# Optimization experiments

Hardware: AMD Instinct MI355X
Metric: run time of the kernel (lower is better)

## Reference

```python
import jax, jax.numpy as jnp
import numpy as np

B, T_H, N, F_P = 16, 24, 256, 6
H, PRED_LEN, F_W = 64, 12, 4


def _build_static(coords):
    # haversine distance matrix -> gaussian kernel -> threshold (epsilon=0.5)
    lon, lat = coords[:, 0], coords[:, 1]
    dlon = lon[None, :] - lon[:, None]
    dlat = lat[None, :] - lat[:, None]
    a = (np.sin(np.radians(dlat / 2)) ** 2
         + np.cos(np.radians(lat[:, None])) * np.cos(np.radians(lat[None, :]))
         * np.sin(np.radians(dlon / 2)) ** 2)
    dist = 2.0 * 6371.0 * np.arcsin(np.sqrt(np.clip(a, 0.0, None)))
    std = dist.flatten().std()
    adj = np.exp(-np.square(dist / std))
    adj[adj < 0.5] = 0.0
    return adj.astype(np.float32)


def setup_inputs() -> dict:
    key = jax.random.key(0)
    ks = jax.random.split(key, 16)
    rng = np.random.default_rng(0)
    coords_np = np.stack([116.0 + rng.uniform(-1.0, 1.0, N),
                          40.0 + rng.uniform(-1.0, 1.0, N)], axis=1).astype(np.float32)
    s = 0.05
    scale_w = jnp.asarray([1.0, 360.0, 10.0, 1.0], jnp.float32)  # [_, dir(deg), speed, _]
    return {
        "history_pollution": jax.random.normal(ks[0], (B, T_H, N, F_P), jnp.float32),
        "history_weather": jax.random.uniform(ks[1], (B, T_H, F_W), jnp.float32) * scale_w,
        "static_adj": jnp.asarray(_build_static(coords_np)),
        "coords": jnp.asarray(coords_np),
        "w_gc1": jax.random.normal(ks[2], (H, F_P), jnp.float32) * s,
        "b_gc1": jax.random.normal(ks[3], (H,), jnp.float32) * s,
        "w_gc2": jax.random.normal(ks[4], (H, H), jnp.float32) * s,
        "b_gc2": jax.random.normal(ks[5], (H,), jnp.float32) * s,
        "w_ih": jax.random.normal(ks[6], (3 * H, H), jnp.float32) * s,
        "w_hh": jax.random.normal(ks[7], (3 * H, H), jnp.float32) * s,
        "b_ih": jax.random.normal(ks[8], (3 * H,), jnp.float32) * s,
        "b_hh": jax.random.normal(ks[9], (3 * H,), jnp.float32) * s,
        "w_m1": jax.random.normal(ks[10], (32, H), jnp.float32) * s,
        "b_m1": jax.random.normal(ks[11], (32,), jnp.float32) * s,
        "w_m2": jax.random.normal(ks[12], (F_P, 32), jnp.float32) * s,
        "b_m2": jax.random.normal(ks[13], (F_P,), jnp.float32) * s,
    }


def _forward(history_pollution, history_weather, static_adj, coords,
             w_gc1, b_gc1, w_gc2, b_gc2, w_ih, w_hh, b_ih, b_hh,
             w_m1, b_m1, w_m2, b_m2):
    Bs, Th, Ns, Fp = history_pollution.shape
    dt = history_pollution.dtype
    eye = jnp.eye(Ns, dtype=dt)
    # station pair angles: vecs[i,j] = coords[j] - coords[i]
    vecs = coords[None, :, :] - coords[:, None, :]
    ang = jnp.arctan2(vecs[..., 1], vecs[..., 0])  # [N,N]

    def gconv(x, adj, w, b):
        wt = adj + eye[None]                         # [B,N,N]
        d = 1.0 / (jnp.sqrt(wt.sum(-1)) + 1e-6)      # [B,N]
        norm = d[:, :, None] * wt * d[:, None, :]    # D^-1/2 W D^-1/2
        return jnp.einsum('bij,bjf->bif', norm, x) @ w.T + b

    def gcb(x, w_out, w_in):
        h1 = jax.nn.relu(gconv(x, w_out, w_gc1, b_gc1))
        return jax.nn.relu(gconv(h1, w_in, w_gc2, b_gc2))

    def gru(h, x):                                   # h,x: [B*N,H]
        gi = x @ w_ih.T + b_ih
        gh = h @ w_hh.T + b_hh
        i_r, i_z, i_n = jnp.split(gi, 3, axis=-1)
        h_r, h_z, h_n = jnp.split(gh, 3, axis=-1)
        r = jax.nn.sigmoid(i_r + h_r)
        z = jax.nn.sigmoid(i_z + h_z)
        n = jnp.tanh(i_n + r * h_n)
        return (1.0 - z) * n + z * h

    def mlp(x):
        return jax.nn.relu(x @ w_m1.T + b_m1) @ w_m2.T + b_m2

    def enc_step(carry, xs):
        h, _ = carry
        x_t, spd, wd = xs                            # [B,N,F],[B],[B]
        rad = jnp.deg2rad(wd)
        w_dyn = jnp.maximum(spd[:, None, None] * jnp.cos(ang[None] - rad[:, None, None]), 0.0)
        w_out = static_adj[None] * w_dyn             # [B,N,N]
        sf = gcb(x_t, w_out, jnp.swapaxes(w_out, 1, 2))
        h = gru(h, sf.reshape(Bs * Ns, -1))
        return (h, w_out), None

    h0 = jnp.zeros((Bs * Ns, w_hh.shape[1]), dt)
    xs = (jnp.moveaxis(history_pollution, 1, 0),      # [T,B,N,F]
          history_weather[:, :, 2].T,                 # wind speed [T,B]
          history_weather[:, :, 1].T)                 # wind dir   [T,B]
    (h, last_w_out), _ = jax.lax.scan(enc_step, (h0, jnp.zeros((Bs, Ns, Ns), dt)), xs)
    last_w_in = jnp.swapaxes(last_w_out, 1, 2)

    dec0 = mlp(h.reshape(Bs, Ns, -1))

    def dec_step(carry, _):
        h_c, x = carry
        sf = gcb(x, last_w_out, last_w_in)
        h_c = gru(h_c, sf.reshape(Bs * Ns, -1))
        pred = mlp(h_c.reshape(Bs, Ns, -1))
        return (h_c, pred), pred

    _, preds = jax.lax.scan(dec_step, (h, dec0), None, length=PRED_LEN)
    return jnp.moveaxis(preds, 0, 1)                  # [B, pred_len, N, F_P]


def reference(history_pollution, history_weather, static_adj, coords,
              w_gc1, b_gc1, w_gc2, b_gc2, w_ih, w_hh, b_ih, b_hh,
              w_m1, b_m1, w_m2, b_m2):
    return _forward(history_pollution, history_weather, static_adj, coords,
                    w_gc1, b_gc1, w_gc2, b_gc2, w_ih, w_hh, b_ih, b_hh,
                    w_m1, b_m1, w_m2, b_m2)
```

## Files before the change

### kernel.cpp

```cpp
#include <hip/hip_runtime.h>
#include <math.h>

#define Bsz 16
#define Tt 24
#define Nn 256
#define Fp 6
#define Hh 64
#define PredL 12
#define Fw 4
#define M1 32
#define TCHUNK 8
#define DEG2RAD 0.017453292519943295f
#define IDX2(t, b) ((t) * Bsz + (b))

__global__ __launch_bounds__(256) void k_prep(
    const float* __restrict__ coords, const float* __restrict__ adj,
    const float* __restrict__ wgc2, const float* __restrict__ wih,
    const float* __restrict__ whh,  const float* __restrict__ wm1,
    const float* __restrict__ wm2,
    float2* __restrict__ pk,
    float* __restrict__ wgc2T, float* __restrict__ wm1T, float* __restrict__ wm2T,
    float4* __restrict__ wihP, float4* __restrict__ whhP) {
  int tid = threadIdx.x;
  if (blockIdx.x < Nn) {
    int i = blockIdx.x;
    int j = tid;
    float dx = coords[2 * j]     - coords[2 * i];
    float dy = coords[2 * j + 1] - coords[2 * i + 1];
    float ang = atan2f(dy, dx);
    float a = adj[i * Nn + j];
    pk[i * Nn + j] = make_float2(a * cosf(ang), a * sinf(ang));
    return;
  }
  for (int idx = tid; idx < Hh * Hh; idx += 256) {
    int g = idx / Hh, k = idx % Hh;
    wgc2T[k * Hh + g] = wgc2[g * Hh + k];
  }
  for (int idx = tid; idx < M1 * Hh; idx += 256) {
    int m = idx / Hh, k = idx % Hh;
    wm1T[k * M1 + m] = wm1[m * Hh + k];
  }
  for (int idx = tid; idx < Fp * M1; idx += 256) {
    int f = idx / M1, m = idx % M1;
    wm2T[m * Fp + f] = wm2[f * M1 + m];
  }
  for (int idx = tid; idx < Hh * 64; idx += 256) {
    int k = idx >> 6, lane = idx & 63;
    wihP[idx] = make_float4(wih[(0 * 64 + lane) * Hh + k],
                            wih[(1 * 64 + lane) * Hh + k],
                            wih[(2 * 64 + lane) * Hh + k], 0.f);
    whhP[idx] = make_float4(whh[(0 * 64 + lane) * Hh + k],
                            whh[(1 * 64 + lane) * Hh + k],
                            whh[(2 * 64 + lane) * Hh + k], 0.f);
  }
}

__global__ __launch_bounds__(256) void k_deg(
    const float* __restrict__ hw, const float2* __restrict__ pk,
    float* __restrict__ dbuf, float* __restrict__ ebuf) {
  int q  = blockIdx.x & 3;
  int tb = blockIdx.x >> 2;
  int t = tb / Bsz, b = tb % Bsz;
  float spd = hw[(b * Tt + t) * Fw + 2];
  float rad = hw[(b * Tt + t) * Fw + 1] * DEG2RAD;
  float cr = cosf(rad), sr = sinf(rad);
  int w = threadIdx.x >> 6, lane = threadIdx.x & 63;
  for (int m = 0; m < 16; ++m) {
    int i = q * 64 + w * 16 + m;
    float rs = 0.f, cs = 0.f;
#pragma unroll
    for (int c = 0; c < 4; ++c) {
      int j = lane + 64 * c;
      float2 pv = pk[i * Nn + j];
      float val = spd * (pv.x * cr + pv.y * sr);
      rs += fmaxf(val, 0.f);
      cs += (j == i) ? fmaxf(val, 0.f) : fmaxf(-val, 0.f);
    }
#pragma unroll
    for (int off = 32; off; off >>= 1) {
      rs += __shfl_xor(rs, off);
      cs += __shfl_xor(cs, off);
    }
    if (lane == 0) {
      dbuf[IDX2(t, b) * Nn + i] = 1.f / (sqrtf(rs + 1.f) + 1e-6f);
      ebuf[IDX2(t, b) * Nn + i] = 1.f / (sqrtf(cs + 1.f) + 1e-6f);
    }
  }
}

__global__ __launch_bounds__(256) void k_enc(
    const float2* __restrict__ pk, const float* __restrict__ hp,
    const float* __restrict__ hw,
    const float* __restrict__ dbuf, const float* __restrict__ ebuf,
    const float* __restrict__ wgc1, const float* __restrict__ bgc1,
    const float* __restrict__ wgc2T, const float* __restrict__ bgc2,
    float* __restrict__ sf_all) {
  __shared__ __align__(16) float u_s[Nn * 8];
  __shared__ __align__(16) float h1_s[Nn * 68];
  int tb = blockIdx.x, t = tb / Bsz, b = tb % Bsz;
  int i = threadIdx.x;
  float spd = hw[(b * Tt + t) * Fw + 2];
  float rad = hw[(b * Tt + t) * Fw + 1] * DEG2RAD;
  float cr = cosf(rad), sr = sinf(rad);
  const float* drow = dbuf + IDX2(t, b) * Nn;
  float di = drow[i];
  float ei = ebuf[IDX2(t, b) * Nn + i];
  const float* xsrc = hp + (long)(b * Tt + t) * Nn * Fp;
  for (int idx = i; idx < Nn * Fp; idx += 256) {
    int j = idx / Fp, f = idx - j * Fp;
    u_s[j * 8 + f] = drow[j] * xsrc[idx];
  }
  u_s[i * 8 + 6] = 0.f;
  u_s[i * 8 + 7] = 0.f;
  __syncthreads();

  float a0 = 0.f, a1 = 0.f, a2 = 0.f, a3 = 0.f, a4 = 0.f, a5 = 0.f;
#pragma unroll 4
  for (int j = 0; j < Nn; ++j) {
    float2 pv = pk[j * Nn + i];
    float vji = spd * (pv.x * cr + pv.y * sr);
    float wout = (j == i) ? fmaxf(vji, 0.f) : fmaxf(-vji, 0.f);
    float4 ul = *(const float4*)&u_s[j * 8];
    float4 uh = *(const float4*)&u_s[j * 8 + 4];
    a0 += wout * ul.x; a1 += wout * ul.y; a2 += wout * ul.z;
    a3 += wout * ul.w; a4 += wout * uh.x; a5 += wout * uh.y;
  }
  float y0 = di * (a0 + u_s[i * 8 + 0]);
  float y1 = di * (a1 + u_s[i * 8 + 1]);
  float y2v = di * (a2 + u_s[i * 8 + 2]);
  float y3 = di * (a3 + u_s[i * 8 + 3]);
  float y4 = di * (a4 + u_s[i * 8 + 4]);
  float y5 = di * (a5 + u_s[i * 8 + 5]);

#pragma unroll
  for (int g4 = 0; g4 < 16; ++g4) {
    float4 hv;
#pragma unroll
    for (int q = 0; q < 4; ++q) {
      int g = g4 * 4 + q;
      float v = bgc1[g] + wgc1[g * Fp + 0] * y0 + wgc1[g * Fp + 1] * y1 +
                wgc1[g * Fp + 2] * y2v + wgc1[g * Fp + 3] * y3 +
                wgc1[g * Fp + 4] * y4 + wgc1[g * Fp + 5] * y5;
      v = fmaxf(v, 0.f) * ei;
      ((float*)&hv)[q] = v;
    }
    *(float4*)&h1_s[i * 68 + g4 * 4] = hv;
  }
  __syncthreads();

  float z[64];
#pragma unroll
  for (int k = 0; k < 64; ++k) z[k] = 0.f;
#pragma unroll 2
  for (int j = 0; j < Nn; ++j) {
    float2 pv = pk[j * Nn + i];
    float vji = spd * (pv.x * cr + pv.y * sr);
    float wf = fmaxf(vji, 0.f) + ((j == i) ? 1.f : 0.f);
#pragma unroll
    for (int g4 = 0; g4 < 16; ++g4) {
      float4 h4 = *(const float4*)&h1_s[j * 68 + g4 * 4];
      z[g4 * 4 + 0] += wf * h4.x;
      z[g4 * 4 + 1] += wf * h4.y;
      z[g4 * 4 + 2] += wf * h4.z;
      z[g4 * 4 + 3] += wf * h4.w;
    }
  }
#pragma unroll
  for (int k = 0; k < 64; ++k) z[k] *= ei;
  __syncthreads();

#pragma unroll
  for (int c = 0; c < 4; ++c) {
    float s[16];
#pragma unroll
    for (int q = 0; q < 16; ++q) s[q] = bgc2[c * 16 + q];
#pragma unroll
    for (int k = 0; k < 64; ++k) {
      float zk = z[k];
#pragma unroll
      for (int q = 0; q < 16; ++q) s[q] += wgc2T[k * Hh + c * 16 + q] * zk;
    }
#pragma unroll
    for (int q4 = 0; q4 < 4; ++q4) {
      float4 sv = make_float4(fmaxf(s[q4 * 4 + 0], 0.f), fmaxf(s[q4 * 4 + 1], 0.f),
                              fmaxf(s[q4 * 4 + 2], 0.f), fmaxf(s[q4 * 4 + 3], 0.f));
      *(float4*)&h1_s[i * 68 + c * 16 + q4 * 4] = sv;
    }
  }
  __syncthreads();
  long base = (long)IDX2(t, b) * Nn * Hh;
  for (int idx = i; idx < Nn * 16; idx += 256) {
    int j = idx >> 4, g4 = idx & 15;
    *(float4*)&sf_all[base + j * Hh + g4 * 4] = *(const float4*)&h1_s[j * 68 + g4 * 4];
  }
}

__global__ __launch_bounds__(256) void k_gi(
    const float* __restrict__ sf_all, const float4* __restrict__ wihP,
    const float* __restrict__ bih, float* __restrict__ gi, int t0) {
  __shared__ float sf_c[4][16][64];
  int tid = threadIdx.x, w = tid >> 6, lane = tid & 63;
  int rowc0 = blockIdx.x * 64 + w * 16;
  long rowg0 = (long)t0 * (Bsz * Nn) + rowc0;
#pragma unroll
  for (int rr = 0; rr < 16; ++rr)
    sf_c[w][rr][lane] = sf_all[(rowg0 + rr) * Hh + lane];
  float bi_r = bih[lane], bi_z = bih[64 + lane], bi_n = bih[128 + lane];
  float ar[16], az[16], an[16];
#pragma unroll
  for (int rr = 0; rr < 16; ++rr) { ar[rr] = bi_r; az[rr] = bi_z; an[rr] = bi_n; }
#pragma unroll 2
  for (int kb = 0; kb < 16; ++kb) {
    int k0 = kb * 4;
    float4 wi0 = wihP[(k0 + 0) * 64 + lane];
    float4 wi1 = wihP[(k0 + 1) * 64 + lane];
    float4 wi2 = wihP[(k0 + 2) * 64 + lane];
    float4 wi3 = wihP[(k0 + 3) * 64 + lane];
#pragma unroll
    for (int rr = 0; rr < 16; ++rr) {
      const float4 s4 = *(const float4*)&sf_c[w][rr][k0];
      ar[rr] += s4.x * wi0.x + s4.y * wi1.x + s4.z * wi2.x + s4.w * wi3.x;
      az[rr] += s4.x * wi0.y + s4.y * wi1.y + s4.z * wi2.y + s4.w * wi3.y;
      an[rr] += s4.x * wi0.z + s4.y * wi1.z + s4.z * wi2.z + s4.w * wi3.z;
    }
  }
#pragma unroll
  for (int rr = 0; rr < 16; ++rr) {
    long rowc = rowc0 + rr;
    gi[(rowc * 3 + 0) * 64 + lane] = ar[rr];
    gi[(rowc * 3 + 1) * 64 + lane] = az[rr];
    gi[(rowc * 3 + 2) * 64 + lane] = an[rr];
  }
}

__global__ __launch_bounds__(256) void k_gru_scan4(
    const float* __restrict__ gi, const float4* __restrict__ whhP,
    const float* __restrict__ bhh, float* __restrict__ hstate,
    int t0, int nt) {
  __shared__ float h_s[16][64];
  int b = blockIdx.x >> 4;
  int i0 = (blockIdx.x & 15) * 16;
  int tid = threadIdx.x, w = tid >> 6, lane = tid & 63;
  float bh_r = bhh[lane], bh_z = bhh[64 + lane], bh_n = bhh[128 + lane];
  float h_reg[4];
#pragma unroll
  for (int rr = 0; rr < 4; ++rr) {
    float hv = (t0 == 0) ? 0.f
                         : hstate[((long)b * Nn + i0 + w * 4 + rr) * Hh + lane];
    h_reg[rr] = hv;
    h_s[w * 4 + rr][lane] = hv;
  }
  for (int tl = 0; tl < nt; ++tl) {
    long rbase = ((long)tl * Bsz + b) * Nn + i0 + w * 4;
    float gr[4], gz[4], gn[4], hr[4], hz[4], hn[4];
#pragma unroll
    for (int rr = 0; rr < 4; ++rr) {
      gr[rr] = gi[((rbase + rr) * 3 + 0) * 64 + lane];
      gz[rr] = gi[((rbase + rr) * 3 + 1) * 64 + lane];
      gn[rr] = gi[((rbase + rr) * 3 + 2) * 64 + lane];
      hr[rr] = bh_r; hz[rr] = bh_z; hn[rr] = bh_n;
    }
#pragma unroll 4
    for (int kb = 0; kb < 16; ++kb) {
      int k0 = kb * 4;
      float4 wh0 = whhP[(k0 + 0) * 64 + lane];
      float4 wh1 = whhP[(k0 + 1) * 64 + lane];
      float4 wh2 = whhP[(k0 + 2) * 64 + lane];
      float4 wh3 = whhP[(k0 + 3) * 64 + lane];
#pragma unroll
      for (int rr = 0; rr < 4; ++rr) {
        const float4 h4 = *(const float4*)&h_s[w * 4 + rr][k0];
        hr[rr] += h4.x * wh0.x + h4.y * wh1.x + h4.z * wh2.x + h4.w * wh3.x;
        hz[rr] += h4.x * wh0.y + h4.y * wh1.y + h4.z * wh2.y + h4.w * wh3.y;
        hn[rr] += h4.x * wh0.z + h4.y * wh1.z + h4.z * wh2.z + h4.w * wh3.z;
      }
    }
#pragma unroll
    for (int rr = 0; rr < 4; ++rr) {
      float rg = 1.f / (1.f + expf(-(gr[rr] + hr[rr])));
      float zg = 1.f / (1.f + expf(-(gz[rr] + hz[rr])));
      float ng = tanhf(gn[rr] + rg * hn[rr]);
      float hv = (1.f - zg) * ng + zg * h_reg[rr];
      h_reg[rr] = hv;
      h_s[w * 4 + rr][lane] = hv;
    }
  }
#pragma unroll
  for (int rr = 0; rr < 4; ++rr)
    hstate[((long)b * Nn + i0 + w * 4 + rr) * Hh + lane] = h_reg[rr];
}

__global__ __launch_bounds__(256) void k_norm_dec(
    const float* __restrict__ hw, const float2* __restrict__ pk,
    const float* __restrict__ dbuf, const float* __restrict__ ebuf,
    float* __restrict__ A1d, float* __restrict__ A2d) {
  int b = blockIdx.x >> 8;
  int i = blockIdx.x & 255;
  int j = threadIdx.x;
  float spd = hw[(b * Tt + (Tt - 1)) * Fw + 2];
  float rad = hw[(b * Tt + (Tt - 1)) * Fw + 1] * DEG2RAD;
  float cr = cosf(rad), sr = sinf(rad);
  const float* drow = dbuf + IDX2(Tt - 1, b) * Nn;
  const float* erow = ebuf + IDX2(Tt - 1, b) * Nn;
  float2 pv = pk[i * Nn + j];
  float val = spd * (pv.x * cr + pv.y * sr);
  float dlt = (j == i) ? 1.f : 0.f;
  float wout = fmaxf(val, 0.f);
  float win  = (j == i) ? wout : fmaxf(-val, 0.f);
  A1d[((long)b * Nn + i) * Nn + j] = drow[i] * (wout + dlt) * drow[j];
  A2d[((long)b * Nn + i) * Nn + j] = erow[i] * (win + dlt) * erow[j];
}

__global__ __launch_bounds__(256) void k_dec0(
    const float* __restrict__ hstate,
    const float* __restrict__ wm1T, const float* __restrict__ bm1,
    const float* __restrict__ wm2T, const float* __restrict__ bm2,
    float* __restrict__ xnext) {
  const int RPB = 16;
  __shared__ float h_lds[RPB][Hh];
  __shared__ float u_lds[RPB][M1];
  int r0 = blockIdx.x * RPB;
  int tid = threadIdx.x;
#pragma unroll
  for (int c = 0; c < (RPB * Hh) / 256; ++c) {
    int idx = tid + c * 256;
    h_lds[idx >> 6][idx & 63] = hstate[(long)r0 * Hh + idx];
  }
  __syncthreads();
#pragma unroll
  for (int rep = 0; rep < 2; ++rep) {
    int idx = tid + rep * 256;
    int row = idx >> 5, m = idx & 31;
    float um = bm1[m];
    for (int k = 0; k < Hh; ++k) um += wm1T[k * M1 + m] * h_lds[row][k];
    u_lds[row][m] = fmaxf(um, 0.f);
  }
  __syncthreads();
  if (tid < RPB * Fp) {
    int row = tid / Fp, f = tid % Fp;
    float pf = bm2[f];
#pragma unroll
    for (int m = 0; m < M1; ++m) pf += wm2T[m * Fp + f] * u_lds[row][m];
    xnext[(r0 + row) * Fp + f] = pf;
  }
}

__global__ __launch_bounds__(256) void k_dstep_A(
    const float* __restrict__ xb, const float* __restrict__ A1d,
    const float* __restrict__ wgc1, const float* __restrict__ bgc1,
    float* __restrict__ h1d) {
  __shared__ float x_lds[Nn * Fp];
  int b = blockIdx.x >> 4;
  int i0 = (blockIdx.x & 15) * 16;
  int tid = threadIdx.x, w = tid >> 6, lane = tid & 63;
  const float* xsrc = xb + (long)b * Nn * Fp;
#pragma unroll
  for (int c = 0; c < 6; ++c) x_lds[tid + 256 * c] = xsrc[tid + 256 * c];
  __syncthreads();
#pragma unroll
  for (int rr = 0; rr < 4; ++rr) {
    int i = i0 + w * 4 + rr;
    const float* arow = A1d + ((long)b * Nn + i) * Nn;
    float acc[Fp] = {0.f, 0.f, 0.f, 0.f, 0.f, 0.f};
#pragma unroll
    for (int c = 0; c < 4; ++c) {
      int j = lane + 64 * c;
      float wt = arow[j];
#pragma unroll
      for (int f = 0; f < Fp; ++f) acc[f] += wt * x_lds[j * Fp + f];
    }
#pragma unroll
    for (int f = 0; f < Fp; ++f) {
#pragma unroll
      for (int off = 32; off; off >>= 1) acc[f] += __shfl_xor(acc[f], off);
    }
    float hv = bgc1[lane];
#pragma unroll
    for (int f = 0; f < Fp; ++f) hv += wgc1[lane * Fp + f] * acc[f];
    h1d[((long)b * Nn + i) * Hh + lane] = fmaxf(hv, 0.f);
  }
}

__global__ __launch_bounds__(256) void k_dstep_B(
    const float* __restrict__ A2d, const float* __restrict__ h1d,
    const float* __restrict__ wgc2T, const float* __restrict__ bgc2,
    const float4* __restrict__ wihP, const float4* __restrict__ whhP,
    const float* __restrict__ bih, const float* __restrict__ bhh,
    float* __restrict__ hstate,
    const float* __restrict__ wm1T, const float* __restrict__ bm1,
    const float* __restrict__ wm2T, const float* __restrict__ bm2,
    float* __restrict__ outp, float* __restrict__ xnext, int p) {
  __shared__ __align__(16) float wvT[Nn * 20];
  __shared__ float red[4][16][Hh];
  __shared__ float y2[16][Hh];
  __shared__ float sf_s[16][Hh];
  __shared__ float h_s[16][Hh];
  __shared__ float hn_lds[16][Hh];
  __shared__ float u_lds[16][M1];
  int b = blockIdx.x >> 4;
  int i0 = (blockIdx.x & 15) * 16;
  int tid = threadIdx.x, w = tid >> 6, lane = tid & 63;

#pragma unroll
  for (int r = 0; r < 16; ++r)
    wvT[tid * 20 + r] = A2d[((long)b * Nn + i0 + r) * Nn + tid];
  float hp_reg[4];
#pragma unroll
  for (int rr = 0; rr < 4; ++rr) {
    hp_reg[rr] = hstate[((long)b * Nn + i0 + w * 4 + rr) * Hh + lane];
    h_s[w * 4 + rr][lane] = hp_reg[rr];
  }
  __syncthreads();

  float acc[16];
#pragma unroll
  for (int r = 0; r < 16; ++r) acc[r] = 0.f;
  const float* h1b = h1d + (long)b * Nn * Hh;
#pragma unroll 4
  for (int jj = 0; jj < 64; ++jj) {
    int j = w * 64 + jj;
    float hv = h1b[j * Hh + lane];
    const float4* wp = (const float4*)(wvT + j * 20);
    float4 w0 = wp[0], w1 = wp[1], w2 = wp[2], w3 = wp[3];
    acc[0] += w0.x * hv; acc[1] += w0.y * hv; acc[2] += w0.z * hv; acc[3] += w0.w * hv;
    acc[4] += w1.x * hv; acc[5] += w1.y * hv; acc[6] += w1.z * hv; acc[7] += w1.w * hv;
    acc[8] += w2.x * hv; acc[9] += w2.y * hv; acc[10] += w2.z * hv; acc[11] += w2.w * hv;
    acc[12] += w3.x * hv; acc[13] += w3.y * hv; acc[14] += w3.z * hv; acc[15] += w3.w * hv;
  }
#pragma unroll
  for (int r = 0; r < 16; ++r) red[w][r][lane] = acc[r];
  __syncthreads();
#pragma unroll
  for (int rr = 0; rr < 4; ++rr) {
    int r = w * 4 + rr;
    y2[r][lane] = red[0][r][lane] + red[1][r][lane] + red[2][r][lane] + red[3][r][lane];
  }
  {
    float a0 = bgc2[lane], a1 = a0, a2 = a0, a3 = a0;
    for (int k = 0; k < Hh; ++k) {
      float wk = wgc2T[k * Hh + lane];
      a0 += wk * y2[w * 4 + 0][k];
      a1 += wk * y2[w * 4 + 1][k];
      a2 += wk * y2[w * 4 + 2][k];
      a3 += wk * y2[w * 4 + 3][k];
    }
    sf_s[w * 4 + 0][lane] = fmaxf(a0, 0.f);
    sf_s[w * 4 + 1][lane] = fmaxf(a1, 0.f);
    sf_s[w * 4 + 2][lane] = fmaxf(a2, 0.f);
    sf_s[w * 4 + 3][lane] = fmaxf(a3, 0.f);
  }

  float hn_reg[4];
  {
    float bi_r = bih[lane], bi_z = bih[64 + lane], bi_n = bih[128 + lane];
    float bh_r = bhh[lane], bh_z = bhh[64 + lane], bh_n = bhh[128 + lane];
    float gir[4], giz[4], gin[4], ghr[4], ghz[4], ghn[4];
#pragma unroll
    for (int rr = 0; rr < 4; ++rr) {
      gir[rr] = bi_r; giz[rr] = bi_z; gin[rr] = bi_n;
      ghr[rr] = bh_r; ghz[rr] = bh_z; ghn[rr] = bh_n;
    }
#pragma unroll 4
    for (int kb = 0; kb < 16; ++kb) {
      int k0 = kb * 4;
      float4 wi[4], wh[4];
#pragma unroll
      for (int q = 0; q < 4; ++q) {
        wi[q] = wihP[(k0 + q) * 64 + lane];
        wh[q] = whhP[(k0 + q) * 64 + lane];
      }
#pragma unroll
      for (int rr = 0; rr < 4; ++rr) {
        const float4 s4 = *(const float4*)&sf_s[w * 4 + rr][k0];
        const float4 h4 = *(const float4*)&h_s[w * 4 + rr][k0];
        gir[rr] += s4.x * wi[0].x + s4.y * wi[1].x + s4.z * wi[2].x + s4.w * wi[3].x;
        giz[rr] += s4.x * wi[0].y + s4.y * wi[1].y + s4.z * wi[2].y + s4.w * wi[3].y;
        gin[rr] += s4.x * wi[0].z + s4.y * wi[1].z + s4.z * wi[2].z + s4.w * wi[3].z;
        ghr[rr] += h4.x * wh[0].x + h4.y * wh[1].x + h4.z * wh[2].x + h4.w * wh[3].x;
        ghz[rr] += h4.x * wh[0].y + h4.y * wh[1].y + h4.z * wh[2].y + h4.w * wh[3].y;
        ghn[rr] += h4.x * wh[0].z + h4.y * wh[1].z + h4.z * wh[2].z + h4.w * wh[3].z;
      }
    }
#pragma unroll
    for (int rr = 0; rr < 4; ++rr) {
      float rg = 1.f / (1.f + expf(-(gir[rr] + ghr[rr])));
      float zg = 1.f / (1.f + expf(-(giz[rr] + ghz[rr])));
      float ng = tanhf(gin[rr] + rg * ghn[rr]);
      hn_reg[rr] = (1.f - zg) * ng + zg * hp_reg[rr];
      hstate[((long)b * Nn + i0 + w * 4 + rr) * Hh + lane] = hn_reg[rr];
      hn_lds[w * 4 + rr][lane] = hn_reg[rr];
    }
  }
  __syncthreads();
#pragma unroll
  for (int rep = 0; rep < 2; ++rep) {
    int idx = tid + rep * 256;
    int row = idx >> 5, m = idx & 31;
    float um = bm1[m];
    for (int k = 0; k < Hh; ++k) um += wm1T[k * M1 + m] * hn_lds[row][k];
    u_lds[row][m] = fmaxf(um, 0.f);
  }
  __syncthreads();
  if (tid < 16 * Fp) {
    int row = tid / Fp, f = tid % Fp;
    float pf = bm2[f];
#pragma unroll
    for (int m = 0; m < M1; ++m) pf += wm2T[m * Fp + f] * u_lds[row][m];
    int i = i0 + row;
    outp[(((long)b * PredL + p) * Nn + i) * Fp + f] = pf;
    xnext[((long)b * Nn + i) * Fp + f] = pf;
  }
}

extern "C" void kernel_launch(void* const* d_in, const int* in_sizes, int n_in,
                              void* d_out, int out_size, void* d_ws, size_t ws_size,
                              hipStream_t stream) {
  const float* hp     = (const float*)d_in[0];
  const float* hw     = (const float*)d_in[1];
  const float* adj    = (const float*)d_in[2];
  const float* coords = (const float*)d_in[3];
  const float* wgc1   = (const float*)d_in[4];
  const float* bgc1   = (const float*)d_in[5];
  const float* wgc2   = (const float*)d_in[6];
  const float* bgc2   = (const float*)d_in[7];
  const float* wih    = (const float*)d_in[8];
  const float* whh    = (const float*)d_in[9];
  const float* bih    = (const float*)d_in[10];
  const float* bhh    = (const float*)d_in[11];
  const float* wm1    = (const float*)d_in[12];
  const float* bm1    = (const float*)d_in[13];
  const float* wm2    = (const float*)d_in[14];
  const float* bm2    = (const float*)d_in[15];
  float* out = (float*)d_out;

  float* w = (float*)d_ws;
  float2* pk    = (float2*)w; w += Nn * Nn * 2;
  float* dbuf   = w; w += Tt * Bsz * Nn;
  float* ebuf   = w; w += Tt * Bsz * Nn;
  float* hstate = w; w += Bsz * Nn * Hh;
  float* sf_all = w; w += (long)Tt * Bsz * Nn * Hh;
  float* gi_ch  = w; w += (long)TCHUNK * Bsz * Nn * 3 * 64;
  float* h1d    = w; w += Bsz * Nn * Hh;
  float* xb0    = w; w += Bsz * Nn * Fp;
  float* xb1    = w; w += Bsz * Nn * Fp;
  float* A1d    = w; w += Bsz * Nn * Nn;
  float* A2d    = w; w += Bsz * Nn * Nn;
  float* wgc2T  = w; w += Hh * Hh;
  float* wm1T   = w; w += Hh * M1;
  float* wm2T   = w; w += M1 * Fp;
  float4* wihP  = (float4*)w; w += Hh * 64 * 4;
  float4* whhP  = (float4*)w; w += Hh * 64 * 4;

  k_prep<<<Nn + 1, 256, 0, stream>>>(coords, adj, wgc2, wih, whh, wm1, wm2,
                                     pk, wgc2T, wm1T, wm2T, wihP, whhP);
  k_deg<<<Tt * Bsz * 4, 256, 0, stream>>>(hw, pk, dbuf, ebuf);

  k_enc<<<Tt * Bsz, 256, 0, stream>>>(pk, hp, hw, dbuf, ebuf,
                                      wgc1, bgc1, wgc2T, bgc2, sf_all);

  for (int s = 0; s < Tt / TCHUNK; ++s) {
    int t0 = s * TCHUNK;
    k_gi<<<(TCHUNK * Bsz * Nn) / 64, 256, 0, stream>>>(sf_all, wihP, bih,
                                                       gi_ch, t0);
    k_gru_scan4<<<Bsz * 16, 256, 0, stream>>>(gi_ch, whhP, bhh, hstate,
                                              t0, TCHUNK);
  }

  k_norm_dec<<<Bsz * Nn, 256, 0, stream>>>(hw, pk, dbuf, ebuf, A1d, A2d);
  k_dec0<<<Bsz * Nn / 16, 256, 0, stream>>>(hstate, wm1T, bm1, wm2T, bm2, xb0);

  for (int p = 0; p < PredL; ++p) {
    float* xin  = (p & 1) ? xb1 : xb0;
    float* xout = (p & 1) ? xb0 : xb1;
    k_dstep_A<<<Bsz * 16, 256, 0, stream>>>(xin, A1d, wgc1, bgc1, h1d);
    k_dstep_B<<<Bsz * 16, 256, 0, stream>>>(
        A2d, h1d, wgc2T, bgc2, wihP, whhP, bih, bhh, hstate,
        wm1T, bm1, wm2T, bm2, out, xout, p);
  }
}
```

Baseline: 738.5 us.

## Fuse degree computation into encoder and register-tile the second graph aggregation

Drops the separate degree kernel and computes the row and column degree normalisers inside each encoder block, keeping only the last timestep's values for the decoder. The second aggregation is restructured so each thread accumulates an 8x8 tile of nodes by features with vectorised pk loads, replacing the per-thread 64-wide accumulator. The final linear layer writes straight to global memory, and the encoder chunk size rises from 8 to 12, which means fewer gi/GRU launches but a larger gi buffer. Degrees are now recomputed in every block, the diagonal term is handled separately, and launch bounds now ask for two blocks per CU.

```diff
diff --git a/kernel.cpp b/kernel.cpp
--- a/kernel.cpp
+++ b/kernel.cpp
@@ -9,7 +9,7 @@
 #define PredL 12
 #define Fw 4
 #define M1 32
-#define TCHUNK 8
+#define TCHUNK 12
 #define DEG2RAD 0.017453292519943295f
 #define IDX2(t, b) ((t) * Bsz + (b))
 
@@ -55,143 +55,174 @@
   }
 }
 
-__global__ __launch_bounds__(256) void k_deg(
-    const float* __restrict__ hw, const float2* __restrict__ pk,
-    float* __restrict__ dbuf, float* __restrict__ ebuf) {
-  int q  = blockIdx.x & 3;
-  int tb = blockIdx.x >> 2;
-  int t = tb / Bsz, b = tb % Bsz;
-  float spd = hw[(b * Tt + t) * Fw + 2];
-  float rad = hw[(b * Tt + t) * Fw + 1] * DEG2RAD;
-  float cr = cosf(rad), sr = sinf(rad);
-  int w = threadIdx.x >> 6, lane = threadIdx.x & 63;
-  for (int m = 0; m < 16; ++m) {
-    int i = q * 64 + w * 16 + m;
-    float rs = 0.f, cs = 0.f;
-#pragma unroll
-    for (int c = 0; c < 4; ++c) {
-      int j = lane + 64 * c;
-      float2 pv = pk[i * Nn + j];
-      float val = spd * (pv.x * cr + pv.y * sr);
-      rs += fmaxf(val, 0.f);
-      cs += (j == i) ? fmaxf(val, 0.f) : fmaxf(-val, 0.f);
-    }
-#pragma unroll
-    for (int off = 32; off; off >>= 1) {
-      rs += __shfl_xor(rs, off);
-      cs += __shfl_xor(cs, off);
-    }
-    if (lane == 0) {
-      dbuf[IDX2(t, b) * Nn + i] = 1.f / (sqrtf(rs + 1.f) + 1e-6f);
-      ebuf[IDX2(t, b) * Nn + i] = 1.f / (sqrtf(cs + 1.f) + 1e-6f);
-    }
-  }
-}
-
-__global__ __launch_bounds__(256) void k_enc(
+__global__ __launch_bounds__(256, 2) void k_enc(
     const float2* __restrict__ pk, const float* __restrict__ hp,
     const float* __restrict__ hw,
-    const float* __restrict__ dbuf, const float* __restrict__ ebuf,
     const float* __restrict__ wgc1, const float* __restrict__ bgc1,
     const float* __restrict__ wgc2T, const float* __restrict__ bgc2,
-    float* __restrict__ sf_all) {
+    float* __restrict__ sf_all,
+    float* __restrict__ d23, float* __restrict__ e23) {
+  __shared__ float d_lds[Nn];
+  __shared__ float e_lds[Nn];
   __shared__ __align__(16) float u_s[Nn * 8];
   __shared__ __align__(16) float h1_s[Nn * 68];
   int tb = blockIdx.x, t = tb / Bsz, b = tb % Bsz;
-  int i = threadIdx.x;
+  int tid = threadIdx.x;
   float spd = hw[(b * Tt + t) * Fw + 2];
   float rad = hw[(b * Tt + t) * Fw + 1] * DEG2RAD;
-  float cr = cosf(rad), sr = sinf(rad);
-  const float* drow = dbuf + IDX2(t, b) * Nn;
-  float di = drow[i];
-  float ei = ebuf[IDX2(t, b) * Nn + i];
-  const float* xsrc = hp + (long)(b * Tt + t) * Nn * Fp;
-  for (int idx = i; idx < Nn * Fp; idx += 256) {
-    int j = idx / Fp, f = idx - j * Fp;
-    u_s[j * 8 + f] = drow[j] * xsrc[idx];
-  }
-  u_s[i * 8 + 6] = 0.f;
-  u_s[i * 8 + 7] = 0.f;
-  __syncthreads();
-
-  float a0 = 0.f, a1 = 0.f, a2 = 0.f, a3 = 0.f, a4 = 0.f, a5 = 0.f;
+  float scr = spd * cosf(rad), ssr = spd * sinf(rad);
+
+  {
+    int i = tid;
+    float rs = 0.f, cs = 0.f;
 #pragma unroll 4
-  for (int j = 0; j < Nn; ++j) {
-    float2 pv = pk[j * Nn + i];
-    float vji = spd * (pv.x * cr + pv.y * sr);
-    float wout = (j == i) ? fmaxf(vji, 0.f) : fmaxf(-vji, 0.f);
-    float4 ul = *(const float4*)&u_s[j * 8];
-    float4 uh = *(const float4*)&u_s[j * 8 + 4];
-    a0 += wout * ul.x; a1 += wout * ul.y; a2 += wout * ul.z;
-    a3 += wout * ul.w; a4 += wout * uh.x; a5 += wout * uh.y;
-  }
-  float y0 = di * (a0 + u_s[i * 8 + 0]);
-  float y1 = di * (a1 + u_s[i * 8 + 1]);
-  float y2v = di * (a2 + u_s[i * 8 + 2]);
-  float y3 = di * (a3 + u_s[i * 8 + 3]);
-  float y4 = di * (a4 + u_s[i * 8 + 4]);
-  float y5 = di * (a5 + u_s[i * 8 + 5]);
-
-#pragma unroll
-  for (int g4 = 0; g4 < 16; ++g4) {
-    float4 hv;
-#pragma unroll
-    for (int q = 0; q < 4; ++q) {
-      int g = g4 * 4 + q;
-      float v = bgc1[g] + wgc1[g * Fp + 0] * y0 + wgc1[g * Fp + 1] * y1 +
-                wgc1[g * Fp + 2] * y2v + wgc1[g * Fp + 3] * y3 +
-                wgc1[g * Fp + 4] * y4 + wgc1[g * Fp + 5] * y5;
-      v = fmaxf(v, 0.f) * ei;
-      ((float*)&hv)[q] = v;
-    }
-    *(float4*)&h1_s[i * 68 + g4 * 4] = hv;
-  }
-  __syncthreads();
-
-  float z[64];
-#pragma unroll
-  for (int k = 0; k < 64; ++k) z[k] = 0.f;
+    for (int j = 0; j < Nn; ++j) {
+      float2 pv = pk[j * Nn + i];
+      float v = pv.x * scr + pv.y * ssr;
+      cs += fmaxf(v, 0.f);
+      rs += fmaxf(-v, 0.f);
+    }
+    float2 pd = pk[i * Nn + i];
+    float vii = pd.x * scr + pd.y * ssr;
+    rs += vii;
+    float di = 1.f / (sqrtf(rs + 1.f) + 1e-6f);
+    float ei = 1.f / (sqrtf(cs + 1.f) + 1e-6f);
+    d_lds[i] = di; e_lds[i] = ei;
+    if (t == Tt - 1) { d23[b * Nn + i] = di; e23[b * Nn + i] = ei; }
+  }
+  __syncthreads();
+
+  {
+    const float* xsrc = hp + (long)(b * Tt + t) * Nn * Fp;
+    for (int idx = tid; idx < Nn * Fp; idx += 256) {
+      int j = idx / Fp, f = idx - j * Fp;
+      u_s[j * 8 + f] = d_lds[j] * xsrc[idx];
+    }
+    u_s[tid * 8 + 6] = 0.f;
+    u_s[tid * 8 + 7] = 0.f;
+  }
+  __syncthreads();
+
+  {
+    int i = tid;
+    float a0 = 0.f, a1 = 0.f, a2 = 0.f, a3 = 0.f, a4 = 0.f, a5 = 0.f;
+#pragma unroll 2
+    for (int j = 0; j < Nn; ++j) {
+      float2 pv = pk[j * Nn + i];
+      float v = pv.x * scr + pv.y * ssr;
+      float w = fmaxf(-v, 0.f);
+      float4 ul = *(const float4*)&u_s[j * 8];
+      float4 uh = *(const float4*)&u_s[j * 8 + 4];
+      a0 += w * ul.x; a1 += w * ul.y; a2 += w * ul.z;
+      a3 += w * ul.w; a4 += w * uh.x; a5 += w * uh.y;
+    }
+    float2 pd = pk[i * Nn + i];
+    float vii = pd.x * scr + pd.y * ssr;
+    float di = d_lds[i], ei = e_lds[i];
+    float c1 = vii + 1.f;
+    float y0 = di * (a0 + c1 * u_s[i * 8 + 0]);
+    float y1 = di * (a1 + c1 * u_s[i * 8 + 1]);
+    float y2 = di * (a2 + c1 * u_s[i * 8 + 2]);
+    float y3 = di * (a3 + c1 * u_s[i * 8 + 3]);
+    float y4 = di * (a4 + c1 * u_s[i * 8 + 4]);
+    float y5 = di * (a5 + c1 * u_s[i * 8 + 5]);
+#pragma unroll
+    for (int g4 = 0; g4 < 16; ++g4) {
+      float4 hv;
+#pragma unroll
+      for (int q = 0; q < 4; ++q) {
+        int g = g4 * 4 + q;
+        float v2 = bgc1[g] + wgc1[g * Fp + 0] * y0 + wgc1[g * Fp + 1] * y1 +
+                   wgc1[g * Fp + 2] * y2 + wgc1[g * Fp + 3] * y3 +
+                   wgc1[g * Fp + 4] * y4 + wgc1[g * Fp + 5] * y5;
+        ((float*)&hv)[q] = fmaxf(v2, 0.f) * ei;
+      }
+      *(float4*)&h1_s[i * 68 + g4 * 4] = hv;
+    }
+  }
+  __syncthreads();
+
+  int gb = tid >> 5, rb = tid & 31;
+  int i0r = rb * 8, g0 = gb * 8;
+  float z[8][8];
+#pragma unroll
+  for (int r = 0; r < 8; ++r)
+#pragma unroll
+    for (int q = 0; q < 8; ++q) z[r][q] = 0.f;
 #pragma unroll 2
   for (int j = 0; j < Nn; ++j) {
-    float2 pv = pk[j * Nn + i];
-    float vji = spd * (pv.x * cr + pv.y * sr);
-    float wf = fmaxf(vji, 0.f) + ((j == i) ? 1.f : 0.f);
-#pragma unroll
-    for (int g4 = 0; g4 < 16; ++g4) {
-      float4 h4 = *(const float4*)&h1_s[j * 68 + g4 * 4];
-      z[g4 * 4 + 0] += wf * h4.x;
-      z[g4 * 4 + 1] += wf * h4.y;
-      z[g4 * 4 + 2] += wf * h4.z;
-      z[g4 * 4 + 3] += wf * h4.w;
-    }
-  }
-#pragma unroll
-  for (int k = 0; k < 64; ++k) z[k] *= ei;
-  __syncthreads();
-
-#pragma unroll
-  for (int c = 0; c < 4; ++c) {
-    float s[16];
-#pragma unroll
-    for (int q = 0; q < 16; ++q) s[q] = bgc2[c * 16 + q];
-#pragma unroll
-    for (int k = 0; k < 64; ++k) {
-      float zk = z[k];
-#pragma unroll
-      for (int q = 0; q < 16; ++q) s[q] += wgc2T[k * Hh + c * 16 + q] * zk;
-    }
-#pragma unroll
-    for (int q4 = 0; q4 < 4; ++q4) {
-      float4 sv = make_float4(fmaxf(s[q4 * 4 + 0], 0.f), fmaxf(s[q4 * 4 + 1], 0.f),
-                              fmaxf(s[q4 * 4 + 2], 0.f), fmaxf(s[q4 * 4 + 3], 0.f));
-      *(float4*)&h1_s[i * 68 + c * 16 + q4 * 4] = sv;
-    }
-  }
-  __syncthreads();
-  long base = (long)IDX2(t, b) * Nn * Hh;
-  for (int idx = i; idx < Nn * 16; idx += 256) {
-    int j = idx >> 4, g4 = idx & 15;
-    *(float4*)&sf_all[base + j * Hh + g4 * 4] = *(const float4*)&h1_s[j * 68 + g4 * 4];
+    float4 hA = *(const float4*)&h1_s[j * 68 + g0];
+    float4 hB = *(const float4*)&h1_s[j * 68 + g0 + 4];
+    const float4* pkr = (const float4*)(pk + (long)j * Nn + i0r);
+    float4 p0 = pkr[0], p1 = pkr[1], p2 = pkr[2], p3 = pkr[3];
+    float wv[8];
+    wv[0] = fmaxf(p0.x * scr + p0.y * ssr, 0.f);
+    wv[1] = fmaxf(p0.z * scr + p0.w * ssr, 0.f);
+    wv[2] = fmaxf(p1.x * scr + p1.y * ssr, 0.f);
+    wv[3] = fmaxf(p1.z * scr + p1.w * ssr, 0.f);
+    wv[4] = fmaxf(p2.x * scr + p2.y * ssr, 0.f);
+    wv[5] = fmaxf(p2.z * scr + p2.w * ssr, 0.f);
+    wv[6] = fmaxf(p3.x * scr + p3.y * ssr, 0.f);
+    wv[7] = fmaxf(p3.z * scr + p3.w * ssr, 0.f);
+#pragma unroll
+    for (int r = 0; r < 8; ++r) {
+      z[r][0] += wv[r] * hA.x; z[r][1] += wv[r] * hA.y;
+      z[r][2] += wv[r] * hA.z; z[r][3] += wv[r] * hA.w;
+      z[r][4] += wv[r] * hB.x; z[r][5] += wv[r] * hB.y;
+      z[r][6] += wv[r] * hB.z; z[r][7] += wv[r] * hB.w;
+    }
+  }
+#pragma unroll
+  for (int r = 0; r < 8; ++r) {
+    int i = i0r + r;
+    float4 hA = *(const float4*)&h1_s[i * 68 + g0];
+    float4 hB = *(const float4*)&h1_s[i * 68 + g0 + 4];
+    float ei = e_lds[i];
+    z[r][0] = (z[r][0] + hA.x) * ei; z[r][1] = (z[r][1] + hA.y) * ei;
+    z[r][2] = (z[r][2] + hA.z) * ei; z[r][3] = (z[r][3] + hA.w) * ei;
+    z[r][4] = (z[r][4] + hB.x) * ei; z[r][5] = (z[r][5] + hB.y) * ei;
+    z[r][6] = (z[r][6] + hB.z) * ei; z[r][7] = (z[r][7] + hB.w) * ei;
+  }
+  __syncthreads();
+#pragma unroll
+  for (int r = 0; r < 8; ++r) {
+    *(float4*)&h1_s[(i0r + r) * 68 + g0] =
+        make_float4(z[r][0], z[r][1], z[r][2], z[r][3]);
+    *(float4*)&h1_s[(i0r + r) * 68 + g0 + 4] =
+        make_float4(z[r][4], z[r][5], z[r][6], z[r][7]);
+  }
+  __syncthreads();
+
+  {
+    int i = tid;
+    float4 zr[16];
+#pragma unroll
+    for (int k4 = 0; k4 < 16; ++k4)
+      zr[k4] = *(const float4*)&h1_s[i * 68 + k4 * 4];
+    long base = (long)IDX2(t, b) * Nn * Hh + (long)i * Hh;
+#pragma unroll
+    for (int c = 0; c < 4; ++c) {
+      float s[16];
+#pragma unroll
+      for (int q = 0; q < 16; ++q) s[q] = bgc2[c * 16 + q];
+#pragma unroll
+      for (int k4 = 0; k4 < 16; ++k4) {
+#pragma unroll
+        for (int e = 0; e < 4; ++e) {
+          int k = k4 * 4 + e;
+          float zk = ((const float*)&zr[k4])[e];
+#pragma unroll
+          for (int q = 0; q < 16; ++q)
+            s[q] += wgc2T[k * Hh + c * 16 + q] * zk;
+        }
+      }
+#pragma unroll
+      for (int q4 = 0; q4 < 4; ++q4) {
+        float4 sv = make_float4(fmaxf(s[q4 * 4 + 0], 0.f), fmaxf(s[q4 * 4 + 1], 0.f),
+                                fmaxf(s[q4 * 4 + 2], 0.f), fmaxf(s[q4 * 4 + 3], 0.f));
+        *(float4*)&sf_all[base + c * 16 + q4 * 4] = sv;
+      }
+    }
   }
 }
 
@@ -292,7 +323,7 @@
 
 __global__ __launch_bounds__(256) void k_norm_dec(
     const float* __restrict__ hw, const float2* __restrict__ pk,
-    const float* __restrict__ dbuf, const float* __restrict__ ebuf,
+    const float* __restrict__ d23, const float* __restrict__ e23,
     float* __restrict__ A1d, float* __restrict__ A2d) {
   int b = blockIdx.x >> 8;
   int i = blockIdx.x & 255;
@@ -300,8 +331,8 @@
   float spd = hw[(b * Tt + (Tt - 1)) * Fw + 2];
   float rad = hw[(b * Tt + (Tt - 1)) * Fw + 1] * DEG2RAD;
   float cr = cosf(rad), sr = sinf(rad);
-  const float* drow = dbuf + IDX2(Tt - 1, b) * Nn;
-  const float* erow = ebuf + IDX2(Tt - 1, b) * Nn;
+  const float* drow = d23 + b * Nn;
+  const float* erow = e23 + b * Nn;
   float2 pv = pk[i * Nn + j];
   float val = spd * (pv.x * cr + pv.y * sr);
   float dlt = (j == i) ? 1.f : 0.f;
@@ -535,8 +566,8 @@
 
   float* w = (float*)d_ws;
   float2* pk    = (float2*)w; w += Nn * Nn * 2;
-  float* dbuf   = w; w += Tt * Bsz * Nn;
-  float* ebuf   = w; w += Tt * Bsz * Nn;
+  float* d23    = w; w += Bsz * Nn;
+  float* e23    = w; w += Bsz * Nn;
   float* hstate = w; w += Bsz * Nn * Hh;
   float* sf_all = w; w += (long)Tt * Bsz * Nn * Hh;
   float* gi_ch  = w; w += (long)TCHUNK * Bsz * Nn * 3 * 64;
@@ -553,11 +584,8 @@
 
   k_prep<<<Nn + 1, 256, 0, stream>>>(coords, adj, wgc2, wih, whh, wm1, wm2,
                                      pk, wgc2T, wm1T, wm2T, wihP, whhP);
-  k_deg<<<Tt * Bsz * 4, 256, 0, stream>>>(hw, pk, dbuf, ebuf);
-
-  k_enc<<<Tt * Bsz, 256, 0, stream>>>(pk, hp, hw, dbuf, ebuf,
-                                      wgc1, bgc1, wgc2T, bgc2, sf_all);
-
+  k_enc<<<Tt * Bsz, 256, 0, stream>>>(pk, hp, hw, wgc1, bgc1, wgc2T, bgc2,
+                                      sf_all, d23, e23);
   for (int s = 0; s < Tt / TCHUNK; ++s) {
     int t0 = s * TCHUNK;
     k_gi<<<(TCHUNK * Bsz * Nn) / 64, 256, 0, stream>>>(sf_all, wihP, bih,
@@ -565,8 +593,7 @@
     k_gru_scan4<<<Bsz * 16, 256, 0, stream>>>(gi_ch, whhP, bhh, hstate,
                                               t0, TCHUNK);
   }
-
-  k_norm_dec<<<Bsz * Nn, 256, 0, stream>>>(hw, pk, dbuf, ebuf, A1d, A2d);
+  k_norm_dec<<<Bsz * Nn, 256, 0, stream>>>(hw, pk, d23, e23, A1d, A2d);
   k_dec0<<<Bsz * Nn / 16, 256, 0, stream>>>(hstate, wm1T, bm1, wm2T, bm2, xb0);
 
   for (int p = 0; p < PredL; ++p) {
```

New measurement: 762.6 us. +3.3%, slower.
